# Performance work log

Measured on AMD Instinct MI355X. Metric: run time of the kernel, lower is better.

## Reference

```python
import jax, jax.numpy as jnp
from jax import lax
import numpy as np

BN_EPS = 1e-5

def _bn(x, g, b, m, v):
    # inference-mode BatchNorm1d (running stats)
    return (x - m) * (g / jnp.sqrt(v + BN_EPS)) + b

def _mlp2(x, W1, g, b, m, v, W2):
    # Linear(no bias) -> BN -> ReLU -> (Dropout off in eval) -> Linear(no bias)
    h = jax.nn.relu(_bn(x @ W1.T, g, b, m, v))
    return h @ W2.T

def setup_inputs() -> dict:
    key = jax.random.key(0)
    ks = iter(jax.random.split(key, 40))
    B, N = 1024, 10
    f32 = jnp.float32
    def w(shape, s=0.02):
        return jax.random.normal(next(ks), shape, f32) * s
    def bn_params(c):
        return (jnp.ones((c,), f32), jnp.zeros((c,), f32),
                jax.random.normal(next(ks), (c,), f32) * 0.1,
                jax.random.uniform(next(ks), (c,), f32, 0.5, 1.5))
    inp = {
        'features_object': jax.random.normal(next(ks), (B, N, 1024), f32),
        'bbox': jax.random.uniform(next(ks), (B, N, 4), f32),
        'word_embedding': jax.random.normal(next(ks), (B, N, 300), f32),
        'sentiment': jax.random.normal(next(ks), (B, N, 4096), f32),
        'body': jax.random.normal(next(ks), (B, 2048), f32),
    }
    # mlp_object: 1024 -> 128 -> 128
    inp['W1_o'] = w((128, 1024)); inp['g_o'], inp['b_o'], inp['m_o'], inp['v_o'] = bn_params(128)
    inp['W2_o'] = w((128, 128))
    # mlp_sentiment: 4096 -> 512 -> 128
    inp['W1_s'] = w((512, 4096)); inp['g_s'], inp['b_s'], inp['m_s'], inp['v_s'] = bn_params(512)
    inp['W2_s'] = w((128, 512))
    # mlp_body: 2048 -> 256 -> 128
    inp['W1_b'] = w((256, 2048)); inp['g_b'], inp['b_b'], inp['m_b'], inp['v_b'] = bn_params(256)
    inp['W2_b'] = w((128, 256))
    # channel attention (CBAM-style, in_planes=10, ratio=2): shared MLP 10->5->10
    inp['Wc1'] = w((5, 10), 0.3)
    inp['Wc2'] = w((10, 5), 0.3)
    # spatial attention: Conv1d(2 -> 1, k=7, pad=3, no bias)
    inp['Wsa'] = w((1, 2, 7), 0.3)
    # fc1: 688 -> 256 (with bias) then BN
    inp['Wf'] = w((256, 688)); inp['bf'] = jnp.zeros((256,), f32)
    inp['g_f'], inp['b_f'], inp['m_f'], inp['v_f'] = bn_params(256)
    return inp

def reference(features_object, bbox, word_embedding, sentiment, body,
              W1_o, g_o, b_o, m_o, v_o, W2_o,
              W1_s, g_s, b_s, m_s, v_s, W2_s,
              W1_b, g_b, b_b, m_b, v_b, W2_b,
              Wc1, Wc2, Wsa, Wf, bf, g_f, b_f, m_f, v_f):
    B, N, _ = features_object.shape
    # per-slice MLPs batched into single GEMMs over B*N rows
    obj = _mlp2(features_object.reshape(B * N, -1), W1_o, g_o, b_o, m_o, v_o, W2_o).reshape(B, N, 128)
    sen = _mlp2(sentiment.reshape(B * N, -1), W1_s, g_s, b_s, m_s, v_s, W2_s).reshape(B, N, 128)
    # body is identical across the N repeats (inference BN), compute once and broadcast
    bod = _mlp2(body.reshape(B, -1), W1_b, g_b, b_b, m_b, v_b, W2_b)
    bod = jnp.broadcast_to(bod[:, None, :], (B, N, 128))
    x = jnp.concatenate([obj, bbox, word_embedding, sen, bod], axis=2)  # [B,N,688]
    # channel attention over the N-slice axis
    def ca_mlp(a):  # [B,N] -> [B,N]
        return jax.nn.relu(a @ Wc1.T) @ Wc2.T
    att_c = jax.nn.sigmoid(ca_mlp(x.mean(axis=2)) + ca_mlp(x.max(axis=2)))  # [B,N]
    x = x * att_c[:, :, None]
    # spatial attention along feature axis
    s = jnp.stack([x.mean(axis=1), x.max(axis=1)], axis=1)  # [B,2,688]
    sa = lax.conv_general_dilated(s, Wsa, (1,), [(3, 3)],
                                  dimension_numbers=('NCH', 'OIH', 'NCH'))  # [B,1,688]
    x = x * jax.nn.sigmoid(sa)
    x = x.sum(axis=1)  # [B,688]
    out = jax.nn.relu(_bn(x @ Wf.T + bf, g_f, b_f, m_f, v_f))  # [B,256]
    return out
```

## Files before the change

kernel.cpp:

```cpp
#include <hip/hip_runtime.h>
#include <hip/hip_bf16.h>
#include <math.h>

typedef __attribute__((ext_vector_type(8))) short short8;
typedef __attribute__((ext_vector_type(4))) float floatx4;

static __device__ __forceinline__ unsigned short f2bf(float f) {
    unsigned int u = __float_as_uint(f);
    unsigned int r = (u + 0x7fffu + ((u >> 16) & 1u)) >> 16;
    return (unsigned short)r;
}

static __device__ __forceinline__ unsigned int pk_bf16(float lo, float hi) {
    unsigned int r;
    asm("v_cvt_pk_bf16_f32 %0, %1, %2" : "=v"(r) : "v"(lo), "v"(hi));
    return r;
}

static __device__ __forceinline__ void g2l16(const void* g, void* l) {
    __builtin_amdgcn_global_load_lds(
        (const __attribute__((address_space(1))) unsigned int*)g,
        (__attribute__((address_space(3))) unsigned int*)l,
        16, 0, 0);
}

struct GDesc {
    const float*          Af;
    const unsigned short* Ab;
    const unsigned short* W;
    float*          Cf;
    unsigned short* Cb;
    const float *bias, *g, *b, *m, *v;
    int M, N, K;
    int Kreal;
    int fuse;
    int nbx;
    int block0;
    int nbb;
    int ksplit;
};
struct GArgs { GDesc g[3]; int n; };

__global__ __launch_bounds__(256)
void gemm_grouped(GArgs ga)
{
    __shared__ float          As_f[2][4096];
    __shared__ unsigned short Bs[2][4096];
    unsigned short* As_b = (unsigned short*)&As_f[0][0];

    const int bid = blockIdx.x;
    int gi = 0;
    #pragma unroll
    for (int i = 1; i < 3; ++i)
        if (i < ga.n && bid >= ga.g[i].block0) gi = i;
    const GDesc d = ga.g[gi];

    int local = bid - d.block0;
    {
        const int cpx = (d.nbb * d.ksplit) >> 3;
        local = (local & 7) * cpx + (local >> 3);
    }
    int kc = 0;
    int Kc = d.K;
    if (d.ksplit > 1) {
        Kc = d.K / d.ksplit;
        kc = local / d.nbb;
        local -= kc * d.nbb;
    }
    const int kbeg = kc * Kc;
    const int bx = local % d.nbx;
    const int by = local / d.nbx;
    const int row0 = by * 128;
    const int col0 = bx * 128;

    const int tid  = threadIdx.x;
    const int wave = tid >> 6;
    const int lane = tid & 63;
    const int qd   = lane >> 4;
    const int ln   = lane & 15;
    const int wr   = (wave >> 1) * 64;
    const int wc   = (wave & 1) * 64;

    const int c0 = wave * 128 + lane;
    const int c1 = c0 + 64;
    const int r0 = c0 >> 2, k0 = (((c0 & 3) ^ ((c0 >> 3) & 3))) * 8;
    const int r1 = c1 >> 2, k1 = (((c1 & 3) ^ ((c1 >> 3) & 3))) * 8;

    const int aro  = wave * 32 + (lane >> 3);
    const int acol = ((lane & 7) ^ (lane >> 3)) * 4;

    const bool afp = (d.Af != nullptr);
    const int niter = Kc >> 5;

    floatx4 acc[4][4];
    #pragma unroll
    for (int i = 0; i < 4; ++i)
        #pragma unroll
        for (int j = 0; j < 4; ++j) acc[i][j] = (floatx4){0.f, 0.f, 0.f, 0.f};

    g2l16(d.W + (size_t)(col0 + r0) * d.K + kbeg + k0, &Bs[0][(size_t)wave * 1024]);
    g2l16(d.W + (size_t)(col0 + r1) * d.K + kbeg + k1, &Bs[0][(size_t)wave * 1024 + 512]);
    if (afp) {
        #pragma unroll
        for (int t = 0; t < 4; ++t)
            g2l16(d.Af + (size_t)(row0 + aro + t * 8) * d.Kreal + kbeg + acol,
                  &As_f[0][(size_t)(wave * 4 + t) * 256]);
    } else {
        g2l16(d.Ab + (size_t)(row0 + r0) * d.K + kbeg + k0, As_b + (size_t)wave * 1024);
        g2l16(d.Ab + (size_t)(row0 + r1) * d.K + kbeg + k1, As_b + (size_t)wave * 1024 + 512);
    }
    __syncthreads();

    int cur = 0;
    for (int it = 0; it < niter; ++it) {
        const int nxt = cur ^ 1;
        const bool pf = (it + 1 < niter);

        if (pf) {
            const int kg = kbeg + (it + 1) * 32;
            g2l16(d.W + (size_t)(col0 + r0) * d.K + kg + k0, &Bs[nxt][(size_t)wave * 1024]);
            g2l16(d.W + (size_t)(col0 + r1) * d.K + kg + k1, &Bs[nxt][(size_t)wave * 1024 + 512]);
            if (afp) {
                #pragma unroll
                for (int t = 0; t < 4; ++t)
                    g2l16(d.Af + (size_t)(row0 + aro + t * 8) * d.Kreal + kg + acol,
                          &As_f[nxt][(size_t)(wave * 4 + t) * 256]);
            } else {
                g2l16(d.Ab + (size_t)(row0 + r0) * d.K + kg + k0, As_b + (size_t)nxt * 4096 + wave * 1024);
                g2l16(d.Ab + (size_t)(row0 + r1) * d.K + kg + k1, As_b + (size_t)nxt * 4096 + wave * 1024 + 512);
            }
        }

        short8 a[4], b[4];
        if (afp) {
            #pragma unroll
            for (int i = 0; i < 4; ++i) {
                const int row = wr + i * 16 + ln;
                const int sw  = row & 7;
                float4 v0 = *(const float4*)&As_f[cur][row * 32 + ((qd * 2)     ^ sw) * 4];
                float4 v1 = *(const float4*)&As_f[cur][row * 32 + ((qd * 2 + 1) ^ sw) * 4];
                int4 pk = { (int)pk_bf16(v0.x, v0.y), (int)pk_bf16(v0.z, v0.w),
                            (int)pk_bf16(v1.x, v1.y), (int)pk_bf16(v1.z, v1.w) };
                a[i] = *(short8*)&pk;
            }
        } else {
            #pragma unroll
            for (int i = 0; i < 4; ++i) {
                const int row = wr + i * 16 + ln;
                const int sw  = (row >> 1) & 3;
                a[i] = *(const short8*)&As_b[(size_t)cur * 4096 + row * 32 + (qd ^ sw) * 8];
            }
        }
        #pragma unroll
        for (int j = 0; j < 4; ++j) {
            const int row = wc + j * 16 + ln;
            const int sw  = (row >> 1) & 3;
            b[j] = *(const short8*)&Bs[cur][row * 32 + (qd ^ sw) * 8];
        }
        #pragma unroll
        for (int i = 0; i < 4; ++i)
            #pragma unroll
            for (int j = 0; j < 4; ++j)
                acc[i][j] = __builtin_amdgcn_mfma_f32_16x16x32_bf16(
                                a[i], b[j], acc[i][j], 0, 0, 0);

        __syncthreads();
        cur = nxt;
    }

    if (d.ksplit > 1) {
        #pragma unroll
        for (int j = 0; j < 4; ++j) {
            const int col = col0 + wc + j * 16 + ln;
            #pragma unroll
            for (int i = 0; i < 4; ++i) {
                #pragma unroll
                for (int r = 0; r < 4; ++r) {
                    const int row = row0 + wr + i * 16 + qd * 4 + r;
                    atomicAdd(&d.Cf[(size_t)row * d.N + col], acc[i][j][r]);
                }
            }
        }
        return;
    }

    #pragma unroll
    for (int j = 0; j < 4; ++j) {
        const int col = col0 + wc + j * 16 + ln;
        float add = d.bias ? d.bias[col] : 0.f;
        float scale = 1.f, shift = 0.f;
        if (d.fuse) {
            scale = d.g[col] * rsqrtf(d.v[col] + 1e-5f);
            shift = d.b[col] - d.m[col] * scale;
        }
        #pragma unroll
        for (int i = 0; i < 4; ++i) {
            #pragma unroll
            for (int r = 0; r < 4; ++r) {
                const int row = row0 + wr + i * 16 + qd * 4 + r;
                float vv = acc[i][j][r] + add;
                if (d.fuse) vv = fmaxf(vv * scale + shift, 0.f);
                if (d.Cf) d.Cf[(size_t)row * d.N + col] = vv;
                if (d.Cb) d.Cb[(size_t)row * d.N + col] = f2bf(vv);
            }
        }
    }
}

struct WSeg { const float* src; unsigned short* dst; int Kreal; int Kp; };
struct WArgs { WSeg s[7]; int off[8]; float4* zdst; int zn; };

__global__ __launch_bounds__(256)
void cvt_weights(WArgs wa)
{
    int i = blockIdx.x * 256 + threadIdx.x;
    if (i >= wa.off[7]) {
        int z = i - wa.off[7];
        if (z < wa.zn) wa.zdst[z] = (float4){0.f, 0.f, 0.f, 0.f};
        return;
    }
    int s = 0;
    #pragma unroll
    for (int j = 1; j < 7; ++j) if (i >= wa.off[j]) s = j;
    const WSeg sg = wa.s[s];
    const int li = i - wa.off[s];
    const int r = li / sg.Kp, c = li - r * sg.Kp;
    sg.dst[li] = (c < sg.Kreal) ? f2bf(sg.src[(size_t)r * sg.Kreal + c])
                                : (unsigned short)0;
}

struct FSeg { const float* src; unsigned short* dstb; float* dstf;
              const float *bias, *g, *b, *m, *v; int N; };
struct FArgs { FSeg s[3]; int off[4]; };

__global__ __launch_bounds__(256)
void bn_finalize(FArgs fa)
{
    int i = blockIdx.x * 256 + threadIdx.x;
    if (i >= fa.off[3]) return;
    int s = 0;
    #pragma unroll
    for (int j = 1; j < 3; ++j) if (i >= fa.off[j]) s = j;
    const FSeg sg = fa.s[s];
    const int li = i - fa.off[s];
    const int e = li * 4;
    const int col = e % sg.N;
    float4 vv = *(const float4*)(sg.src + e);
    float4 fo;
    ushort4 o;
    #pragma unroll
    for (int r = 0; r < 4; ++r) {
        float x = (&vv.x)[r];
        if (sg.bias) x += sg.bias[col + r];
        float sc = sg.g[col + r] * rsqrtf(sg.v[col + r] + 1e-5f);
        float sh = sg.b[col + r] - sg.m[col + r] * sc;
        x = fmaxf(x * sc + sh, 0.f);
        (&fo.x)[r] = x;
        ((unsigned short*)&o)[r] = f2bf(x);
    }
    if (sg.dstb) *(ushort4*)(sg.dstb + e) = o;
    if (sg.dstf) *(float4*)(sg.dstf + e) = fo;
}

__global__ __launch_bounds__(256)
void attn_kernel(const float* __restrict__ obj, const float* __restrict__ bbox,
                 const float* __restrict__ word, const float* __restrict__ sen,
                 const float* __restrict__ bod,
                 const float* __restrict__ Wc1, const float* __restrict__ Wc2,
                 const float* __restrict__ Wsa,
                 float* __restrict__ xsum_out)
{
    const int b = blockIdx.x;
    const int tid = threadIdx.x;

    __shared__ float xs[10][688];
    __shared__ float s0[688], s1[688];
    __shared__ float avec[10], mvec[10], att[10];
    __shared__ float cw[14], c1[50], c2[50];

    if (tid < 14) cw[tid] = Wsa[tid];
    if (tid < 50) { c1[tid] = Wc1[tid]; c2[tid] = Wc2[tid]; }

    for (int n = 0; n < 10; ++n) {
        const float* o  = obj  + ((size_t)b * 10 + n) * 128;
        const float* bx = bbox + ((size_t)b * 10 + n) * 4;
        const float* w  = word + ((size_t)b * 10 + n) * 300;
        const float* s  = sen  + ((size_t)b * 10 + n) * 128;
        const float* bo = bod  + (size_t)b * 128;
        for (int c = tid; c < 688; c += 256) {
            float v;
            if      (c < 128) v = o[c];
            else if (c < 132) v = bx[c - 128];
            else if (c < 432) v = w[c - 132];
            else if (c < 560) v = s[c - 432];
            else              v = bo[c - 560];
            xs[n][c] = v;
        }
    }
    __syncthreads();

    {
        const int wv = tid >> 6, ln2 = tid & 63;
        for (int n = wv; n < 10; n += 4) {
            float sm = 0.f, mx = -INFINITY;
            for (int c = ln2; c < 688; c += 64) {
                float v = xs[n][c];
                sm += v; mx = fmaxf(mx, v);
            }
            #pragma unroll
            for (int off = 32; off > 0; off >>= 1) {
                sm += __shfl_down(sm, off);
                mx = fmaxf(mx, __shfl_down(mx, off));
            }
            if (ln2 == 0) { avec[n] = sm * (1.f / 688.f); mvec[n] = mx; }
        }
    }
    __syncthreads();

    if (tid == 0) {
        float ha[5], hm[5];
        #pragma unroll
        for (int i = 0; i < 5; ++i) {
            float sa_ = 0.f, sm_ = 0.f;
            #pragma unroll
            for (int j = 0; j < 10; ++j) {
                sa_ += c1[i * 10 + j] * avec[j];
                sm_ += c1[i * 10 + j] * mvec[j];
            }
            ha[i] = fmaxf(sa_, 0.f);
            hm[i] = fmaxf(sm_, 0.f);
        }
        #pragma unroll
        for (int j = 0; j < 10; ++j) {
            float v = 0.f;
            #pragma unroll
            for (int i = 0; i < 5; ++i) v += c2[j * 5 + i] * (ha[i] + hm[i]);
            att[j] = 1.f / (1.f + expf(-v));
        }
    }
    __syncthreads();

    for (int c = tid; c < 688; c += 256) {
        float sm = 0.f, mx = -INFINITY;
        #pragma unroll
        for (int n = 0; n < 10; ++n) {
            float v = xs[n][c] * att[n];
            xs[n][c] = v;
            sm += v; mx = fmaxf(mx, v);
        }
        s0[c] = sm * 0.1f;
        s1[c] = mx;
    }
    __syncthreads();

    for (int c = tid; c < 688; c += 256) {
        float sa = 0.f;
        #pragma unroll
        for (int j = 0; j < 7; ++j) {
            int cc = c + j - 3;
            if (cc >= 0 && cc < 688)
                sa += cw[j] * s0[cc] + cw[7 + j] * s1[cc];
        }
        float sig = 1.f / (1.f + expf(-sa));
        float sm = 0.f;
        #pragma unroll
        for (int n = 0; n < 10; ++n) sm += xs[n][c];
        xsum_out[(size_t)b * 688 + c] = sm * sig;
    }
}

extern "C" void kernel_launch(void* const* d_in, const int* in_sizes, int n_in,
                              void* d_out, int out_size, void* d_ws, size_t ws_size,
                              hipStream_t stream)
{
    const float* f_obj = (const float*)d_in[0];
    const float* bbox  = (const float*)d_in[1];
    const float* word  = (const float*)d_in[2];
    const float* sent  = (const float*)d_in[3];
    const float* body  = (const float*)d_in[4];
    const float* W1_o  = (const float*)d_in[5];
    const float* g_o = (const float*)d_in[6],  *b_o = (const float*)d_in[7];
    const float* m_o = (const float*)d_in[8],  *v_o = (const float*)d_in[9];
    const float* W2_o  = (const float*)d_in[10];
    const float* W1_s  = (const float*)d_in[11];
    const float* g_s = (const float*)d_in[12], *b_s = (const float*)d_in[13];
    const float* m_s = (const float*)d_in[14], *v_s = (const float*)d_in[15];
    const float* W2_s  = (const float*)d_in[16];
    const float* W1_b  = (const float*)d_in[17];
    const float* g_b = (const float*)d_in[18], *b_b = (const float*)d_in[19];
    const float* m_b = (const float*)d_in[20], *v_b = (const float*)d_in[21];
    const float* W2_b  = (const float*)d_in[22];
    const float* Wc1 = (const float*)d_in[23];
    const float* Wc2 = (const float*)d_in[24];
    const float* Wsa = (const float*)d_in[25];
    const float* Wf  = (const float*)d_in[26];
    const float* bf  = (const float*)d_in[27];
    const float* g_f = (const float*)d_in[28], *b_f = (const float*)d_in[29];
    const float* m_f = (const float*)d_in[30], *v_f = (const float*)d_in[31];
    float* out = (float*)d_out;

    char* p = (char*)d_ws;
    unsigned short* w1s = (unsigned short*)p; p += 4194304;
    unsigned short* w2s = (unsigned short*)p; p += 131072;
    unsigned short* w1o = (unsigned short*)p; p += 262144;
    unsigned short* w2o = (unsigned short*)p; p += 32768;
    unsigned short* w1b = (unsigned short*)p; p += 1048576;
    unsigned short* w2b = (unsigned short*)p; p += 65536;
    unsigned short* wfp = (unsigned short*)p; p += 360448;
    unsigned short* h_s = (unsigned short*)p; p += 10485760;
    unsigned short* h_o = (unsigned short*)p; p += 2621440;
    unsigned short* h_b = (unsigned short*)p; p += 524288;
    char* region = p; p += 27262976;
    float* ps = (float*)region;
    float* po = (float*)(region + 20971520);
    float* pb = (float*)(region + 26214400);
    float* sen_f  = (float*)region;
    float* obj_f  = (float*)(region + 5242880);
    float* bod_f  = (float*)(region + 10485760);
    float* xsum_f = (float*)(region + 11010048);
    if ((size_t)(p - (char*)d_ws) > ws_size) return;

    WArgs wa;
    wa.s[0] = { W1_s, w1s, 4096, 4096 };
    wa.s[1] = { W2_s, w2s,  512,  512 };
    wa.s[2] = { W1_o, w1o, 1024, 1024 };
    wa.s[3] = { W2_o, w2o,  128,  128 };
    wa.s[4] = { W1_b, w1b, 2048, 2048 };
    wa.s[5] = { W2_b, w2b,  256,  256 };
    wa.s[6] = { Wf,   wfp,  688,  704 };
    const int wn[7] = { 512*4096, 128*512, 128*1024, 128*128, 256*2048, 128*256, 256*704 };
    wa.off[0] = 0;
    for (int i = 0; i < 7; ++i) wa.off[i + 1] = wa.off[i] + wn[i];
    wa.zdst = (float4*)region;
    wa.zn   = 27262976 / 16;
    cvt_weights<<<(wa.off[7] + wa.zn + 255) / 256, 256, 0, stream>>>(wa);

    {
        GArgs ga; ga.n = 3;
        ga.g[0] = { sent,  nullptr, w1s, ps, nullptr, nullptr, nullptr, nullptr, nullptr, nullptr,
                    10240, 512, 4096, 4096, 0, 4, 0,   320, 2 };
        ga.g[1] = { f_obj, nullptr, w1o, po, nullptr, nullptr, nullptr, nullptr, nullptr, nullptr,
                    10240, 128, 1024, 1024, 0, 1, 640, 80,  2 };
        ga.g[2] = { body,  nullptr, w1b, pb, nullptr, nullptr, nullptr, nullptr, nullptr, nullptr,
                    1024,  256, 2048, 2048, 0, 2, 800, 16,  2 };
        gemm_grouped<<<832, 256, 0, stream>>>(ga);
    }

    {
        FArgs fa;
        fa.s[0] = { ps, h_s, nullptr, nullptr, g_s, b_s, m_s, v_s, 512 };
        fa.s[1] = { po, h_o, nullptr, nullptr, g_o, b_o, m_o, v_o, 128 };
        fa.s[2] = { pb, h_b, nullptr, nullptr, g_b, b_b, m_b, v_b, 256 };
        fa.off[0] = 0;
        fa.off[1] = 10240 * 512 / 4;
        fa.off[2] = fa.off[1] + 10240 * 128 / 4;
        fa.off[3] = fa.off[2] + 1024 * 256 / 4;
        bn_finalize<<<(fa.off[3] + 255) / 256, 256, 0, stream>>>(fa);
    }

    {
        GArgs ga; ga.n = 3;
        ga.g[0] = { nullptr, h_s, w2s, sen_f, nullptr, nullptr, nullptr, nullptr, nullptr, nullptr,
                    10240, 128, 512, 512, 0, 1, 0,   80, 1 };
        ga.g[1] = { nullptr, h_o, w2o, obj_f, nullptr, nullptr, nullptr, nullptr, nullptr, nullptr,
                    10240, 128, 128, 128, 0, 1, 80,  80, 1 };
        ga.g[2] = { nullptr, h_b, w2b, bod_f, nullptr, nullptr, nullptr, nullptr, nullptr, nullptr,
                    1024,  128, 256, 256, 0, 1, 160, 8,  1 };
        gemm_grouped<<<168, 256, 0, stream>>>(ga);
    }

    attn_kernel<<<1024, 256, 0, stream>>>(obj_f, bbox, word, sen_f, bod_f,
                                          Wc1, Wc2, Wsa, xsum_f);

    {
        GArgs ga; ga.n = 1;
        ga.g[0] = { xsum_f, nullptr, wfp, out, nullptr, bf, g_f, b_f, m_f, v_f,
                    1024, 256, 704, 688, 1, 2, 0, 16, 1 };
        gemm_grouped<<<16, 256, 0, stream>>>(ga);
    }
}
```

Before: 512.5 us.

## Fuse BN-ReLU into second GEMM A-load and fc1 into attention kernel

Removes the separate bn_finalize pass by applying the per-channel BN scale/shift and ReLU as the fp32 first-layer partials are loaded into the second-layer GEMMs, which now read fp32 A and split K in two. The final fc1 GEMM is folded into the attention kernel, where each block does a 688x256 matvec over a k-pair-packed bf16 weight layout and applies bias, BN and ReLU. This cuts two launches and a full round trip of the bf16 hidden activations. In exchange, the second GEMM reads fp32 A from memory, and the per-block fc1 matvec is scalar FMA work rather than MFMA.

```diff
diff --git a/kernel.cpp b/kernel.cpp
--- a/kernel.cpp
+++ b/kernel.cpp
@@ -22,6 +22,15 @@
         (const __attribute__((address_space(1))) unsigned int*)g,
         (__attribute__((address_space(3))) unsigned int*)l,
         16, 0, 0);
+}
+
+static __device__ __forceinline__ float4 bnrelu4(float4 v, float4 s, float4 h) {
+    float4 r;
+    r.x = fmaxf(v.x * s.x + h.x, 0.f);
+    r.y = fmaxf(v.y * s.y + h.y, 0.f);
+    r.z = fmaxf(v.z * s.z + h.z, 0.f);
+    r.w = fmaxf(v.w * s.w + h.w, 0.f);
+    return r;
 }
 
 struct GDesc {
@@ -38,6 +47,7 @@
     int block0;
     int nbb;
     int ksplit;
+    int fuseA;
 };
 struct GArgs { GDesc g[3]; int n; };
 
@@ -46,6 +56,7 @@
 {
     __shared__ float          As_f[2][4096];
     __shared__ unsigned short Bs[2][4096];
+    __shared__ float scL[256], shL[256];
     unsigned short* As_b = (unsigned short*)&As_f[0][0];
 
     const int bid = blockIdx.x;
@@ -98,6 +109,13 @@
         #pragma unroll
         for (int j = 0; j < 4; ++j) acc[i][j] = (floatx4){0.f, 0.f, 0.f, 0.f};
 
+    if (d.fuseA) {
+        for (int k = tid; k < Kc; k += 256) {
+            float sc = d.g[kbeg + k] * rsqrtf(d.v[kbeg + k] + 1e-5f);
+            scL[k] = sc;
+            shL[k] = d.b[kbeg + k] - d.m[kbeg + k] * sc;
+        }
+    }
     g2l16(d.W + (size_t)(col0 + r0) * d.K + kbeg + k0, &Bs[0][(size_t)wave * 1024]);
     g2l16(d.W + (size_t)(col0 + r1) * d.K + kbeg + k1, &Bs[0][(size_t)wave * 1024 + 512]);
     if (afp) {
@@ -133,12 +151,22 @@
 
         short8 a[4], b[4];
         if (afp) {
+            const int kl = it * 32;
             #pragma unroll
             for (int i = 0; i < 4; ++i) {
                 const int row = wr + i * 16 + ln;
                 const int sw  = row & 7;
-                float4 v0 = *(const float4*)&As_f[cur][row * 32 + ((qd * 2)     ^ sw) * 4];
-                float4 v1 = *(const float4*)&As_f[cur][row * 32 + ((qd * 2 + 1) ^ sw) * 4];
+                const int c0f = ((qd * 2)     ^ sw) * 4;
+                const int c1f = ((qd * 2 + 1) ^ sw) * 4;
+                float4 v0 = *(const float4*)&As_f[cur][row * 32 + c0f];
+                float4 v1 = *(const float4*)&As_f[cur][row * 32 + c1f];
+                if (d.fuseA) {
+                    const int kf = kl + qd * 8;
+                    v0 = bnrelu4(v0, *(const float4*)&scL[kf],
+                                     *(const float4*)&shL[kf]);
+                    v1 = bnrelu4(v1, *(const float4*)&scL[kf + 4],
+                                     *(const float4*)&shL[kf + 4]);
+                }
                 int4 pk = { (int)pk_bf16(v0.x, v0.y), (int)pk_bf16(v0.z, v0.w),
                             (int)pk_bf16(v1.x, v1.y), (int)pk_bf16(v1.z, v1.w) };
                 a[i] = *(short8*)&pk;
@@ -207,7 +235,7 @@
     }
 }
 
-struct WSeg { const float* src; unsigned short* dst; int Kreal; int Kp; };
+struct WSeg { const float* src; void* dst; int Kreal; int Kp; };
 struct WArgs { WSeg s[7]; int off[8]; float4* zdst; int zn; };
 
 __global__ __launch_bounds__(256)
@@ -224,42 +252,17 @@
     for (int j = 1; j < 7; ++j) if (i >= wa.off[j]) s = j;
     const WSeg sg = wa.s[s];
     const int li = i - wa.off[s];
+    if (s == 6) {
+        const int k2 = li >> 8, c = li & 255;
+        const int ka = k2 * 2, kb = k2 * 2 + 1;
+        unsigned int lo = (ka < 688) ? f2bf(sg.src[(size_t)c * 688 + ka]) : 0u;
+        unsigned int hi = (kb < 688) ? f2bf(sg.src[(size_t)c * 688 + kb]) : 0u;
+        ((unsigned int*)sg.dst)[li] = lo | (hi << 16);
+        return;
+    }
     const int r = li / sg.Kp, c = li - r * sg.Kp;
-    sg.dst[li] = (c < sg.Kreal) ? f2bf(sg.src[(size_t)r * sg.Kreal + c])
-                                : (unsigned short)0;
-}
-
-struct FSeg { const float* src; unsigned short* dstb; float* dstf;
-              const float *bias, *g, *b, *m, *v; int N; };
-struct FArgs { FSeg s[3]; int off[4]; };
-
-__global__ __launch_bounds__(256)
-void bn_finalize(FArgs fa)
-{
-    int i = blockIdx.x * 256 + threadIdx.x;
-    if (i >= fa.off[3]) return;
-    int s = 0;
-    #pragma unroll
-    for (int j = 1; j < 3; ++j) if (i >= fa.off[j]) s = j;
-    const FSeg sg = fa.s[s];
-    const int li = i - fa.off[s];
-    const int e = li * 4;
-    const int col = e % sg.N;
-    float4 vv = *(const float4*)(sg.src + e);
-    float4 fo;
-    ushort4 o;
-    #pragma unroll
-    for (int r = 0; r < 4; ++r) {
-        float x = (&vv.x)[r];
-        if (sg.bias) x += sg.bias[col + r];
-        float sc = sg.g[col + r] * rsqrtf(sg.v[col + r] + 1e-5f);
-        float sh = sg.b[col + r] - sg.m[col + r] * sc;
-        x = fmaxf(x * sc + sh, 0.f);
-        (&fo.x)[r] = x;
-        ((unsigned short*)&o)[r] = f2bf(x);
-    }
-    if (sg.dstb) *(ushort4*)(sg.dstb + e) = o;
-    if (sg.dstf) *(float4*)(sg.dstf + e) = fo;
+    ((unsigned short*)sg.dst)[li] =
+        (c < sg.Kreal) ? f2bf(sg.src[(size_t)r * sg.Kreal + c]) : (unsigned short)0;
 }
 
 __global__ __launch_bounds__(256)
@@ -268,13 +271,18 @@
                  const float* __restrict__ bod,
                  const float* __restrict__ Wc1, const float* __restrict__ Wc2,
                  const float* __restrict__ Wsa,
-                 float* __restrict__ xsum_out)
+                 const unsigned int* __restrict__ wfpk,
+                 const float* __restrict__ bf,
+                 const float* __restrict__ g_f, const float* __restrict__ b_f,
+                 const float* __restrict__ m_f, const float* __restrict__ v_f,
+                 float* __restrict__ out)
 {
     const int b = blockIdx.x;
     const int tid = threadIdx.x;
 
     __shared__ float xs[10][688];
     __shared__ float s0[688], s1[688];
+    __shared__ float xr[688];
     __shared__ float avec[10], mvec[10], att[10];
     __shared__ float cw[14], c1[50], c2[50];
 
@@ -365,7 +373,22 @@
         float sm = 0.f;
         #pragma unroll
         for (int n = 0; n < 10; ++n) sm += xs[n][c];
-        xsum_out[(size_t)b * 688 + c] = sm * sig;
+        xr[c] = sm * sig;
+    }
+    __syncthreads();
+
+    {
+        float acc = 0.f;
+        #pragma unroll 4
+        for (int k2 = 0; k2 < 344; ++k2) {
+            unsigned int w2 = wfpk[(size_t)k2 * 256 + tid];
+            float wlo = __uint_as_float(w2 << 16);
+            float whi = __uint_as_float(w2 & 0xffff0000u);
+            acc += wlo * xr[2 * k2] + whi * xr[2 * k2 + 1];
+        }
+        float sc = g_f[tid] * rsqrtf(v_f[tid] + 1e-5f);
+        float sh = b_f[tid] - m_f[tid] * sc;
+        out[(size_t)b * 256 + tid] = fmaxf((acc + bf[tid]) * sc + sh, 0.f);
     }
 }
 
@@ -400,82 +423,61 @@
     float* out = (float*)d_out;
 
     char* p = (char*)d_ws;
-    unsigned short* w1s = (unsigned short*)p; p += 4194304;
-    unsigned short* w2s = (unsigned short*)p; p += 131072;
-    unsigned short* w1o = (unsigned short*)p; p += 262144;
-    unsigned short* w2o = (unsigned short*)p; p += 32768;
-    unsigned short* w1b = (unsigned short*)p; p += 1048576;
-    unsigned short* w2b = (unsigned short*)p; p += 65536;
-    unsigned short* wfp = (unsigned short*)p; p += 360448;
-    unsigned short* h_s = (unsigned short*)p; p += 10485760;
-    unsigned short* h_o = (unsigned short*)p; p += 2621440;
-    unsigned short* h_b = (unsigned short*)p; p += 524288;
-    char* region = p; p += 27262976;
-    float* ps = (float*)region;
-    float* po = (float*)(region + 20971520);
-    float* pb = (float*)(region + 26214400);
-    float* sen_f  = (float*)region;
-    float* obj_f  = (float*)(region + 5242880);
-    float* bod_f  = (float*)(region + 10485760);
-    float* xsum_f = (float*)(region + 11010048);
+    unsigned short* w1s  = (unsigned short*)p; p += 4194304;
+    unsigned short* w2s  = (unsigned short*)p; p += 131072;
+    unsigned short* w1o  = (unsigned short*)p; p += 262144;
+    unsigned short* w2o  = (unsigned short*)p; p += 32768;
+    unsigned short* w1b  = (unsigned short*)p; p += 1048576;
+    unsigned short* w2b  = (unsigned short*)p; p += 65536;
+    unsigned int*   wfpk = (unsigned int*)p;   p += 360448;
+    char* zbase = p;
+    float* sen_f = (float*)p; p += 5242880;
+    float* obj_f = (float*)p; p += 5242880;
+    float* bod_f = (float*)p; p += 524288;
+    float* ps    = (float*)p; p += 20971520;
+    float* po    = (float*)p; p += 5242880;
+    float* pb    = (float*)p; p += 1048576;
+    const int zbytes = 38273024;
     if ((size_t)(p - (char*)d_ws) > ws_size) return;
 
     WArgs wa;
-    wa.s[0] = { W1_s, w1s, 4096, 4096 };
-    wa.s[1] = { W2_s, w2s,  512,  512 };
-    wa.s[2] = { W1_o, w1o, 1024, 1024 };
-    wa.s[3] = { W2_o, w2o,  128,  128 };
-    wa.s[4] = { W1_b, w1b, 2048, 2048 };
-    wa.s[5] = { W2_b, w2b,  256,  256 };
-    wa.s[6] = { Wf,   wfp,  688,  704 };
-    const int wn[7] = { 512*4096, 128*512, 128*1024, 128*128, 256*2048, 128*256, 256*704 };
+    wa.s[0] = { W1_s, w1s,  4096, 4096 };
+    wa.s[1] = { W2_s, w2s,   512,  512 };
+    wa.s[2] = { W1_o, w1o,  1024, 1024 };
+    wa.s[3] = { W2_o, w2o,   128,  128 };
+    wa.s[4] = { W1_b, w1b,  2048, 2048 };
+    wa.s[5] = { W2_b, w2b,   256,  256 };
+    wa.s[6] = { Wf,   wfpk,  688,  704 };
+    const int wn[7] = { 512*4096, 128*512, 128*1024, 128*128, 256*2048, 128*256, 352*256 };
     wa.off[0] = 0;
     for (int i = 0; i < 7; ++i) wa.off[i + 1] = wa.off[i] + wn[i];
-    wa.zdst = (float4*)region;
-    wa.zn   = 27262976 / 16;
+    wa.zdst = (float4*)zbase;
+    wa.zn   = zbytes / 16;
     cvt_weights<<<(wa.off[7] + wa.zn + 255) / 256, 256, 0, stream>>>(wa);
 
     {
         GArgs ga; ga.n = 3;
         ga.g[0] = { sent,  nullptr, w1s, ps, nullptr, nullptr, nullptr, nullptr, nullptr, nullptr,
-                    10240, 512, 4096, 4096, 0, 4, 0,   320, 2 };
+                    10240, 512, 4096, 4096, 0, 4, 0,   320, 2, 0 };
         ga.g[1] = { f_obj, nullptr, w1o, po, nullptr, nullptr, nullptr, nullptr, nullptr, nullptr,
-                    10240, 128, 1024, 1024, 0, 1, 640, 80,  2 };
+                    10240, 128, 1024, 1024, 0, 1, 640, 80,  2, 0 };
         ga.g[2] = { body,  nullptr, w1b, pb, nullptr, nullptr, nullptr, nullptr, nullptr, nullptr,
-                    1024,  256, 2048, 2048, 0, 2, 800, 16,  2 };
+                    1024,  256, 2048, 2048, 0, 2, 800, 16,  2, 0 };
         gemm_grouped<<<832, 256, 0, stream>>>(ga);
-    }
-
-    {
-        FArgs fa;
-        fa.s[0] = { ps, h_s, nullptr, nullptr, g_s, b_s, m_s, v_s, 512 };
-        fa.s[1] = { po, h_o, nullptr, nullptr, g_o, b_o, m_o, v_o, 128 };
-        fa.s[2] = { pb, h_b, nullptr, nullptr, g_b, b_b, m_b, v_b, 256 };
-        fa.off[0] = 0;
-        fa.off[1] = 10240 * 512 / 4;
-        fa.off[2] = fa.off[1] + 10240 * 128 / 4;
-        fa.off[3] = fa.off[2] + 1024 * 256 / 4;
-        bn_finalize<<<(fa.off[3] + 255) / 256, 256, 0, stream>>>(fa);
     }
 
     {
         GArgs ga; ga.n = 3;
-        ga.g[0] = { nullptr, h_s, w2s, sen_f, nullptr, nullptr, nullptr, nullptr, nullptr, nullptr,
-                    10240, 128, 512, 512, 0, 1, 0,   80, 1 };
-        ga.g[1] = { nullptr, h_o, w2o, obj_f, nullptr, nullptr, nullptr, nullptr, nullptr, nullptr,
-                    10240, 128, 128, 128, 0, 1, 80,  80, 1 };
-        ga.g[2] = { nullptr, h_b, w2b, bod_f, nullptr, nullptr, nullptr, nullptr, nullptr, nullptr,
-                    1024,  128, 256, 256, 0, 1, 160, 8,  1 };
-        gemm_grouped<<<168, 256, 0, stream>>>(ga);
+        ga.g[0] = { ps, nullptr, w2s, sen_f, nullptr, nullptr, g_s, b_s, m_s, v_s,
+                    10240, 128, 512, 512, 0, 1, 0,   80, 2, 1 };
+        ga.g[1] = { po, nullptr, w2o, obj_f, nullptr, nullptr, g_o, b_o, m_o, v_o,
+                    10240, 128, 128, 128, 0, 1, 160, 80, 2, 1 };
+        ga.g[2] = { pb, nullptr, w2b, bod_f, nullptr, nullptr, g_b, b_b, m_b, v_b,
+                    1024,  128, 256, 256, 0, 1, 320, 8,  2, 1 };
+        gemm_grouped<<<336, 256, 0, stream>>>(ga);
     }
 
     attn_kernel<<<1024, 256, 0, stream>>>(obj_f, bbox, word, sen_f, bod_f,
-                                          Wc1, Wc2, Wsa, xsum_f);
-
-    {
-        GArgs ga; ga.n = 1;
-        ga.g[0] = { xsum_f, nullptr, wfp, out, nullptr, bf, g_f, b_f, m_f, v_f,
-                    1024, 256, 704, 688, 1, 2, 0, 16, 1 };
-        gemm_grouped<<<16, 256, 0, stream>>>(ga);
-    }
-}
+                                          Wc1, Wc2, Wsa, wfpk, bf,
+                                          g_f, b_f, m_f, v_f, out);
+}
```

After: 495.5 us. 3.3% less time.
